# Performance work log

Measured on AMD Instinct MI355X. Metric: run time of the kernel, lower is better.

## Reference

```python
import jax, jax.numpy as jnp
import numpy as np

D_MODEL = 1024
NUM_HEADS = 16
HEAD_DIM = D_MODEL // NUM_HEADS  # 64
ROPE_BASE = 10000.0


def setup_inputs() -> dict:
    key = jax.random.key(0)
    ks = jax.random.split(key, 12)
    B, S, D = 4, 2048, D_MODEL
    scale = 1.0 / np.sqrt(D)
    inp = {
        'query': jax.random.normal(ks[0], (B, S, D), jnp.float32),
        'key': jax.random.normal(ks[1], (B, S, D), jnp.float32),
        'value': jax.random.normal(ks[2], (B, S, D), jnp.float32),
        'Wq': jax.random.normal(ks[3], (D, D), jnp.float32) * scale,
        'bq': jnp.zeros((D,), jnp.float32),
        'Wk': jax.random.normal(ks[4], (D, D), jnp.float32) * scale,
        'bk': jnp.zeros((D,), jnp.float32),
        'Wv': jax.random.normal(ks[5], (D, D), jnp.float32) * scale,
        'bv': jnp.zeros((D,), jnp.float32),
        'Wo': jax.random.normal(ks[6], (D, D), jnp.float32) * scale,
        'bo': jnp.zeros((D,), jnp.float32),
    }
    return inp


def _rope_cos_sin(seq_len, head_dim, dtype):
    inv_freq = 1.0 / (ROPE_BASE ** (jnp.arange(0, head_dim, 2, dtype=jnp.float32) / head_dim))
    t = jnp.arange(seq_len, dtype=jnp.float32)
    freqs = jnp.einsum('i,j->ij', t, inv_freq)          # [S, hd/2]
    emb = jnp.concatenate([freqs, freqs], axis=-1)      # [S, hd]
    return jnp.cos(emb).astype(dtype), jnp.sin(emb).astype(dtype)


def _rotate_half(x):
    x1, x2 = jnp.split(x, 2, axis=-1)
    return jnp.concatenate([-x2, x1], axis=-1)


def reference(query, key, value, Wq, bq, Wk, bk, Wv, bv, Wo, bo):
    B, T, D = query.shape
    H, hd = NUM_HEADS, HEAD_DIM
    # projections -> [B, H, S, hd]
    Q = (query @ Wq + bq).reshape(B, T, H, hd).transpose(0, 2, 1, 3)
    K = (key @ Wk + bk).reshape(B, -1, H, hd).transpose(0, 2, 1, 3)
    V = (value @ Wv + bv).reshape(B, -1, H, hd).transpose(0, 2, 1, 3)
    # RoPE
    cos, sin = _rope_cos_sin(T, hd, Q.dtype)            # [S, hd]
    Q = Q * cos + _rotate_half(Q) * sin
    K = K * cos + _rotate_half(K) * sin
    # attention
    scores = jnp.einsum('bhtd,bhsd->bhts', Q, K) / jnp.sqrt(jnp.asarray(hd, Q.dtype))
    attn = jax.nn.softmax(scores, axis=-1)
    context = jnp.einsum('bhts,bhsd->bhtd', attn, V)
    context = context.transpose(0, 2, 1, 3).reshape(B, T, D)
    return context @ Wo + bo
```

## Files before the change

### kernel.cpp

```cpp
#include <hip/hip_runtime.h>
#include <hip/hip_bf16.h>
#include <cstdint>
#include <cstddef>

typedef __bf16 bf16_t;
typedef __bf16 bf16x8 __attribute__((ext_vector_type(8)));
typedef __bf16 bf16x4v __attribute__((ext_vector_type(4)));
typedef __bf16 bf16x2v __attribute__((ext_vector_type(2)));
typedef float f32x4 __attribute__((ext_vector_type(4)));
typedef float f32x16 __attribute__((ext_vector_type(16)));
typedef uint32_t u32x4 __attribute__((ext_vector_type(4)));

#define DEVI static __device__ __forceinline__

DEVI void gl_lds16(const void* g, void* l) {
    __builtin_amdgcn_global_load_lds((const __attribute__((address_space(1))) void*)g,
                                     (__attribute__((address_space(3))) void*)l, 16, 0, 0);
}

DEVI float fexp2(float x) {
#if __has_builtin(__builtin_amdgcn_exp2f)
    return __builtin_amdgcn_exp2f(x);
#else
    return __expf(x * 0.6931471805599453f);
#endif
}

DEVI uint32_t pkbf16(float a, float b) {
    bf16x2v t;
    t[0] = (bf16_t)a;
    t[1] = (bf16_t)b;
    return __builtin_bit_cast(uint32_t, t);
}

__global__ __launch_bounds__(256) void castk(const float* __restrict__ i0, const float* __restrict__ i1,
                                             const float* __restrict__ i2, bf16_t* __restrict__ o0,
                                             bf16_t* __restrict__ o1, bf16_t* __restrict__ o2) {
    const float* in = blockIdx.y == 0 ? i0 : blockIdx.y == 1 ? i1 : i2;
    bf16_t* out = blockIdx.y == 0 ? o0 : blockIdx.y == 1 ? o1 : o2;
    size_t i = ((size_t)blockIdx.x * 256 + threadIdx.x) * 4;
    float4 v = *(const float4*)(in + i);
    bf16x4v o;
    o[0] = (bf16_t)v.x; o[1] = (bf16_t)v.y; o[2] = (bf16_t)v.z; o[3] = (bf16_t)v.w;
    *(bf16x4v*)(out + i) = o;
}

__global__ __launch_bounds__(256) void wtrans(const float* __restrict__ W0, const float* __restrict__ W1,
                                              const float* __restrict__ W2, const float* __restrict__ W3,
                                              bf16_t* __restrict__ O0, bf16_t* __restrict__ O1,
                                              bf16_t* __restrict__ O2, bf16_t* __restrict__ O3) {
    const float* W; bf16_t* O;
    switch (blockIdx.z) {
        case 0: W = W0; O = O0; break;
        case 1: W = W1; O = O1; break;
        case 2: W = W2; O = O2; break;
        default: W = W3; O = O3; break;
    }
    __shared__ float t[32][33];
    int tx = threadIdx.x & 31, ty = threadIdx.x >> 5;
    int bx = blockIdx.x * 32, by = blockIdx.y * 32;
#pragma unroll
    for (int yy = 0; yy < 4; ++yy)
        t[ty + yy * 8][tx] = W[(size_t)(by + ty + yy * 8) * 1024 + bx + tx];
    __syncthreads();
#pragma unroll
    for (int yy = 0; yy < 4; ++yy)
        O[(size_t)(bx + ty + yy * 8) * 1024 + by + tx] = (bf16_t)t[tx][ty + yy * 8];
}

__global__ __launch_bounds__(256) void rope_tab(float* __restrict__ ctab, float* __restrict__ stab) {
    int idx = blockIdx.x * 256 + threadIdx.x;
    int s = idx >> 5, i = idx & 31;
    float inv = 1.0f / powf(10000.0f, (float)i * (1.0f / 32.0f));
    float f = (float)s * inv;
    ctab[idx] = cosf(f);
    stab[idx] = sinf(f);
}

__global__ __launch_bounds__(256) void gemm_qkv(const bf16_t* __restrict__ Xq, const bf16_t* __restrict__ Xk,
                                                const bf16_t* __restrict__ Xv, const bf16_t* __restrict__ Wqt,
                                                const bf16_t* __restrict__ Wkt, const bf16_t* __restrict__ Wvt,
                                                const float* __restrict__ bqp, const float* __restrict__ bkp,
                                                const float* __restrict__ bvp, bf16_t* __restrict__ Qo,
                                                bf16_t* __restrict__ Ko, bf16_t* __restrict__ Vo,
                                                const float* __restrict__ ctab, const float* __restrict__ stab) {
    constexpr int K = 1024;
    const int z = blockIdx.z;
    const bf16_t* A  = z == 0 ? Xq : z == 1 ? Xk : Xv;
    const bf16_t* Bt = z == 0 ? Wqt : z == 1 ? Wkt : Wvt;
    const float* bias = z == 0 ? bqp : z == 1 ? bkp : bvp;
    bf16_t* O = z == 0 ? Qo : z == 1 ? Ko : Vo;
    const float scale = z == 0 ? 0.18033688011112042f : 1.0f;

    __shared__ alignas(16) bf16_t As[128 * 32];
    __shared__ alignas(16) bf16_t Bs[128 * 32];
    const int tid = threadIdx.x;
    const int w = tid >> 6, lane = tid & 63, c = lane & 15, qd = lane >> 4;
    const int wm = w >> 1, wn = w & 1;
    const int m0 = blockIdx.x * 128, n0 = blockIdx.y * 128;
    f32x4 acc[4][4] = {};
    for (int kt = 0; kt < K / 32; ++kt) {
#pragma unroll
        for (int l = 0; l < 2; ++l) {
            int e = (l * 256 + tid) * 8;
            int row = e >> 5, col = e & 31;
            gl_lds16(A + (size_t)(m0 + row) * K + kt * 32 + col, (char*)As + (size_t)e * 2);
            gl_lds16(Bt + (size_t)(n0 + row) * K + kt * 32 + col, (char*)Bs + (size_t)e * 2);
        }
        __syncthreads();
        bf16x8 af[4], bfr[4];
#pragma unroll
        for (int i = 0; i < 4; ++i) af[i] = *(const bf16x8*)&As[(wm * 64 + i * 16 + c) * 32 + qd * 8];
#pragma unroll
        for (int j = 0; j < 4; ++j) bfr[j] = *(const bf16x8*)&Bs[(wn * 64 + j * 16 + c) * 32 + qd * 8];
#pragma unroll
        for (int i = 0; i < 4; ++i)
#pragma unroll
            for (int j = 0; j < 4; ++j)
                acc[i][j] = __builtin_amdgcn_mfma_f32_16x16x32_bf16(af[i], bfr[j], acc[i][j], 0, 0, 0);
        __syncthreads();
    }
    const int mb = m0 + wm * 64;
    const int nb = n0 + wn * 64;
    const int h = nb >> 6;
    if (z == 2) {
#pragma unroll
        for (int i = 0; i < 4; ++i) {
            int m = mb + i * 16 + qd * 4;
            int b = m >> 11, s = m & 2047;
#pragma unroll
            for (int j = 0; j < 4; ++j) {
                int d = j * 16 + c;
                float bv = bias[nb + d];
                bf16x4v v4;
#pragma unroll
                for (int r = 0; r < 4; ++r) v4[r] = (bf16_t)(acc[i][j][r] + bv);
                *(bf16x4v*)(O + ((size_t)(b * 16 + h) * 64 + d) * 2048 + s) = v4;
            }
        }
    } else {
#pragma unroll
        for (int i = 0; i < 4; ++i)
#pragma unroll
            for (int jh = 0; jh < 2; ++jh) {
                int d1 = jh * 16 + c;
                float b1 = bias[nb + d1];
                float b2 = bias[nb + d1 + 32];
#pragma unroll
                for (int r = 0; r < 4; ++r) {
                    int m = mb + i * 16 + qd * 4 + r;
                    int b = m >> 11, s = m & 2047;
                    float v1 = acc[i][jh][r] + b1;
                    float v2 = acc[i][jh + 2][r] + b2;
                    float ct = ctab[s * 32 + d1];
                    float st = stab[s * 32 + d1];
                    size_t base = ((size_t)(b * 16 + h) * 2048 + s) * 64;
                    O[base + d1]      = (bf16_t)((v1 * ct - v2 * st) * scale);
                    O[base + d1 + 32] = (bf16_t)((v2 * ct + v1 * st) * scale);
                }
            }
    }
}

__global__ __launch_bounds__(256) void gemm_out(const bf16_t* __restrict__ A, const bf16_t* __restrict__ Bt,
                                                const float* __restrict__ bias, float* __restrict__ O) {
    constexpr int K = 1024, N = 1024;
    __shared__ alignas(16) bf16_t As[128 * 32];
    __shared__ alignas(16) bf16_t Bs[128 * 32];
    const int tid = threadIdx.x;
    const int w = tid >> 6, lane = tid & 63, c = lane & 15, qd = lane >> 4;
    const int wm = w >> 1, wn = w & 1;
    const int m0 = blockIdx.x * 128, n0 = blockIdx.y * 128;
    f32x4 acc[4][4] = {};
    for (int kt = 0; kt < K / 32; ++kt) {
#pragma unroll
        for (int l = 0; l < 2; ++l) {
            int e = (l * 256 + tid) * 8;
            int row = e >> 5, col = e & 31;
            gl_lds16(A + (size_t)(m0 + row) * K + kt * 32 + col, (char*)As + (size_t)e * 2);
            gl_lds16(Bt + (size_t)(n0 + row) * K + kt * 32 + col, (char*)Bs + (size_t)e * 2);
        }
        __syncthreads();
        bf16x8 af[4], bfr[4];
#pragma unroll
        for (int i = 0; i < 4; ++i) af[i] = *(const bf16x8*)&As[(wm * 64 + i * 16 + c) * 32 + qd * 8];
#pragma unroll
        for (int j = 0; j < 4; ++j) bfr[j] = *(const bf16x8*)&Bs[(wn * 64 + j * 16 + c) * 32 + qd * 8];
#pragma unroll
        for (int i = 0; i < 4; ++i)
#pragma unroll
            for (int j = 0; j < 4; ++j)
                acc[i][j] = __builtin_amdgcn_mfma_f32_16x16x32_bf16(af[i], bfr[j], acc[i][j], 0, 0, 0);
        __syncthreads();
    }
    const int mb = m0 + wm * 64, nb = n0 + wn * 64;
#pragma unroll
    for (int i = 0; i < 4; ++i)
#pragma unroll
        for (int j = 0; j < 4; ++j) {
            int n = nb + j * 16 + c;
            float bv = bias[n];
#pragma unroll
            for (int r = 0; r < 4; ++r) {
                int m = mb + i * 16 + qd * 4 + r;
                O[(size_t)m * N + n] = acc[i][j][r] + bv;
            }
        }
}

__global__ __launch_bounds__(256) void attn(const bf16_t* __restrict__ Q, const bf16_t* __restrict__ K,
                                            const bf16_t* __restrict__ Vt, bf16_t* __restrict__ ctx) {
    constexpr int S = 2048;
    __shared__ alignas(16) char smem[32768];
    const int tid = threadIdx.x, w = tid >> 6, lane = tid & 63;
    const int lo5 = lane & 31, hi = lane >> 5;
    const int rm = (lo5 >> 1) & 7;
    const int bh = blockIdx.x, q0 = blockIdx.y * 256;
    const bf16_t* Qb = Q + (size_t)bh * S * 64 + (size_t)q0 * 64;
    const bf16_t* Kb = K + (size_t)bh * S * 64;
    const bf16_t* Vb = Vt + (size_t)bh * 64 * S;
#pragma unroll
    for (int l = 0; l < 8; ++l) {
        int slot = l * 256 + tid;
        int row = slot >> 3, ch = slot & 7;
        int sch = ch ^ ((row >> 1) & 7);
        gl_lds16(Qb + (size_t)row * 64 + sch * 8, smem + (size_t)slot * 16);
    }
    __syncthreads();
    bf16x8 qf[4][2];
    {
        const bf16_t* Qs = (const bf16_t*)smem;
#pragma unroll
        for (int kc = 0; kc < 4; ++kc)
#pragma unroll
            for (int qb = 0; qb < 2; ++qb)
                qf[kc][qb] = *(const bf16x8*)&Qs[(size_t)(w * 64 + qb * 32 + lo5) * 64 + ((kc * 2 + hi) ^ rm) * 8];
    }
    __syncthreads();
    auto stageKV = [&](int kt, int buf) {
        const int s0 = kt * 64;
        char* kbase = smem + buf * 16384;
        char* vbase = kbase + 8192;
#pragma unroll
        for (int l = 0; l < 2; ++l) {
            int slot = l * 256 + tid;
            int row = slot >> 3, ch = slot & 7;
            int sch = ch ^ ((row >> 1) & 7);
            gl_lds16(Kb + (size_t)(s0 + row) * 64 + sch * 8, kbase + (size_t)slot * 16);
            gl_lds16(Vb + (size_t)row * S + s0 + sch * 8, vbase + (size_t)slot * 16);
        }
    };
    stageKV(0, 0);
    f32x16 acc_o[2][2] = {};
    f32x16 acc_l[2] = {};
    const f32x16 Z16 = {};
    bf16x8 ones;
    {
        u32x4 ov = {0x3F803F80u, 0x3F803F80u, 0x3F803F80u, 0x3F803F80u};
        ones = __builtin_bit_cast(bf16x8, ov);
    }
    __syncthreads();
    for (int kt = 0; kt < S / 64; ++kt) {
        const int cur = kt & 1;
        if (kt + 1 < S / 64) stageKV(kt + 1, cur ^ 1);
        const bf16_t* KsC = (const bf16_t*)(smem + cur * 16384);
        const bf16_t* VsC = (const bf16_t*)(smem + cur * 16384 + 8192);
        f32x16 st[2][2];
#pragma unroll
        for (int kc = 0; kc < 4; ++kc) {
            bf16x8 kf[2];
#pragma unroll
            for (int sb = 0; sb < 2; ++sb)
                kf[sb] = *(const bf16x8*)&KsC[(size_t)(sb * 32 + lo5) * 64 + ((kc * 2 + hi) ^ rm) * 8];
#pragma unroll
            for (int sb = 0; sb < 2; ++sb)
#pragma unroll
                for (int qb = 0; qb < 2; ++qb)
                    st[sb][qb] = __builtin_amdgcn_mfma_f32_32x32x16_bf16(kf[sb], qf[kc][qb],
                                                                         kc == 0 ? Z16 : st[sb][qb], 0, 0, 0);
        }
        uint32_t pku[2][2][8];
#pragma unroll
        for (int sb = 0; sb < 2; ++sb)
#pragma unroll
            for (int qb = 0; qb < 2; ++qb)
#pragma unroll
                for (int u = 0; u < 8; ++u)
                    pku[sb][qb][u] = pkbf16(fexp2(st[sb][qb][2 * u]), fexp2(st[sb][qb][2 * u + 1]));
#pragma unroll
        for (int skc = 0; skc < 4; ++skc) {
            bf16x8 vf[2];
#pragma unroll
            for (int db = 0; db < 2; ++db)
                vf[db] = *(const bf16x8*)&VsC[(size_t)(db * 32 + lo5) * 64 + ((skc * 2 + hi) ^ rm) * 8];
            const int sb = skc >> 1, b = (skc & 1) * 4;
#pragma unroll
            for (int qb = 0; qb < 2; ++qb) {
                uint32_t p0 = pku[sb][qb][b + 0], p1 = pku[sb][qb][b + 1];
                uint32_t p2 = pku[sb][qb][b + 2], p3 = pku[sb][qb][b + 3];
                uint32_t send0 = hi ? p0 : p2;
                uint32_t send1 = hi ? p1 : p3;
                uint32_t recv0 = __shfl_xor(send0, 32);
                uint32_t recv1 = __shfl_xor(send1, 32);
                u32x4 av = {hi ? recv0 : p0, hi ? recv1 : p1,
                            hi ? p2 : recv0, hi ? p3 : recv1};
                bf16x8 af = __builtin_bit_cast(bf16x8, av);
                acc_l[qb] = __builtin_amdgcn_mfma_f32_32x32x16_bf16(af, ones, acc_l[qb], 0, 0, 0);
#pragma unroll
                for (int db = 0; db < 2; ++db)
                    acc_o[qb][db] = __builtin_amdgcn_mfma_f32_32x32x16_bf16(af, vf[db], acc_o[qb][db], 0, 0, 0);
            }
        }
        __syncthreads();
    }
    const int b = bh >> 4, h = bh & 15;
#pragma unroll
    for (int qb = 0; qb < 2; ++qb) {
        float linv[16];
#pragma unroll
        for (int r = 0; r < 16; ++r) linv[r] = 1.0f / acc_l[qb][r];
#pragma unroll
        for (int db = 0; db < 2; ++db)
#pragma unroll
            for (int r = 0; r < 16; ++r) {
                int qrow = q0 + w * 64 + qb * 32 + (r & 3) + 8 * (r >> 2) + 4 * hi;
                int d = db * 32 + lo5;
                float o = acc_o[qb][db][r] * linv[r];
                ctx[((size_t)(b * 2048 + qrow)) * 1024 + (size_t)h * 64 + d] = (bf16_t)o;
            }
    }
}

extern "C" void kernel_launch(void* const* d_in, const int* in_sizes, int n_in,
                              void* d_out, int out_size, void* d_ws, size_t ws_size,
                              hipStream_t stream) {
    (void)in_sizes; (void)n_in; (void)out_size; (void)ws_size;
    const float* query = (const float*)d_in[0];
    const float* key   = (const float*)d_in[1];
    const float* value = (const float*)d_in[2];
    const float* Wq = (const float*)d_in[3];
    const float* bq = (const float*)d_in[4];
    const float* Wk = (const float*)d_in[5];
    const float* bk = (const float*)d_in[6];
    const float* Wv = (const float*)d_in[7];
    const float* bv = (const float*)d_in[8];
    const float* Wo = (const float*)d_in[9];
    const float* bo = (const float*)d_in[10];

    const size_t SZ = (size_t)8192 * 1024;
    bf16_t* Xq = (bf16_t*)d_ws;
    bf16_t* Xk = Xq + SZ;
    bf16_t* Xv = Xk + SZ;
    bf16_t* Qb = Xv + SZ;
    bf16_t* Kb = Qb + SZ;
    bf16_t* Vtb = Kb + SZ;
    bf16_t* Wqt = Vtb + SZ;
    bf16_t* Wkt = Wqt + 1024 * 1024;
    bf16_t* Wvt = Wkt + 1024 * 1024;
    bf16_t* Wot = Wvt + 1024 * 1024;
    float* ctab = (float*)(Wot + 1024 * 1024);
    float* stab = ctab + 2048 * 32;
    bf16_t* CT = Xq;

    castk<<<dim3(8192, 3), 256, 0, stream>>>(query, key, value, Xq, Xk, Xv);
    wtrans<<<dim3(32, 32, 4), 256, 0, stream>>>(Wq, Wk, Wv, Wo, Wqt, Wkt, Wvt, Wot);
    rope_tab<<<256, 256, 0, stream>>>(ctab, stab);
    gemm_qkv<<<dim3(64, 8, 3), 256, 0, stream>>>(Xq, Xk, Xv, Wqt, Wkt, Wvt, bq, bk, bv,
                                                 Qb, Kb, Vtb, ctab, stab);
    attn<<<dim3(64, 8), 256, 0, stream>>>(Qb, Kb, Vtb, CT);
    gemm_out<<<dim3(64, 8), 256, 0, stream>>>(CT, Wot, bo, (float*)d_out);
}
```

Before: 359.5 us.

## Halve attention query tile per block and use permlane32_swap for P exchange

The attention kernel now handles 128 query rows per block (32 per wave) instead of 256, which halves the per-wave accumulators and Q fragments and doubles the grid to 1024 blocks, with launch bounds requesting 4 blocks per CU. This is meant to raise occupancy and fill more CUs on the MI355X. In exchange, K/V tiles are streamed through LDS twice as often per query row, and each K/V fragment read feeds fewer MFMAs. The lane exchange of the P operand also uses the permlane32_swap builtin when available, replacing shuffles and selects.

```diff
diff --git a/kernel.cpp b/kernel.cpp
--- a/kernel.cpp
+++ b/kernel.cpp
@@ -10,6 +10,7 @@
 typedef float f32x4 __attribute__((ext_vector_type(4)));
 typedef float f32x16 __attribute__((ext_vector_type(16)));
 typedef uint32_t u32x4 __attribute__((ext_vector_type(4)));
+typedef uint32_t u32x2 __attribute__((ext_vector_type(2)));
 
 #define DEVI static __device__ __forceinline__
 
@@ -208,33 +209,31 @@
         }
 }
 
-__global__ __launch_bounds__(256) void attn(const bf16_t* __restrict__ Q, const bf16_t* __restrict__ K,
-                                            const bf16_t* __restrict__ Vt, bf16_t* __restrict__ ctx) {
+__global__ __launch_bounds__(256, 4) void attn(const bf16_t* __restrict__ Q, const bf16_t* __restrict__ K,
+                                               const bf16_t* __restrict__ Vt, bf16_t* __restrict__ ctx) {
     constexpr int S = 2048;
     __shared__ alignas(16) char smem[32768];
     const int tid = threadIdx.x, w = tid >> 6, lane = tid & 63;
     const int lo5 = lane & 31, hi = lane >> 5;
     const int rm = (lo5 >> 1) & 7;
-    const int bh = blockIdx.x, q0 = blockIdx.y * 256;
+    const int bh = blockIdx.x, q0 = blockIdx.y * 128;
     const bf16_t* Qb = Q + (size_t)bh * S * 64 + (size_t)q0 * 64;
     const bf16_t* Kb = K + (size_t)bh * S * 64;
     const bf16_t* Vb = Vt + (size_t)bh * 64 * S;
 #pragma unroll
-    for (int l = 0; l < 8; ++l) {
+    for (int l = 0; l < 4; ++l) {
         int slot = l * 256 + tid;
         int row = slot >> 3, ch = slot & 7;
         int sch = ch ^ ((row >> 1) & 7);
         gl_lds16(Qb + (size_t)row * 64 + sch * 8, smem + (size_t)slot * 16);
     }
     __syncthreads();
-    bf16x8 qf[4][2];
+    bf16x8 qf[4];
     {
         const bf16_t* Qs = (const bf16_t*)smem;
 #pragma unroll
         for (int kc = 0; kc < 4; ++kc)
-#pragma unroll
-            for (int qb = 0; qb < 2; ++qb)
-                qf[kc][qb] = *(const bf16x8*)&Qs[(size_t)(w * 64 + qb * 32 + lo5) * 64 + ((kc * 2 + hi) ^ rm) * 8];
+            qf[kc] = *(const bf16x8*)&Qs[(size_t)(w * 32 + lo5) * 64 + ((kc * 2 + hi) ^ rm) * 8];
     }
     __syncthreads();
     auto stageKV = [&](int kt, int buf) {
@@ -251,8 +250,8 @@
         }
     };
     stageKV(0, 0);
-    f32x16 acc_o[2][2] = {};
-    f32x16 acc_l[2] = {};
+    f32x16 acc_o[2] = {};
+    f32x16 acc_l = {};
     const f32x16 Z16 = {};
     bf16x8 ones;
     {
@@ -265,7 +264,7 @@
         if (kt + 1 < S / 64) stageKV(kt + 1, cur ^ 1);
         const bf16_t* KsC = (const bf16_t*)(smem + cur * 16384);
         const bf16_t* VsC = (const bf16_t*)(smem + cur * 16384 + 8192);
-        f32x16 st[2][2];
+        f32x16 st[2];
 #pragma unroll
         for (int kc = 0; kc < 4; ++kc) {
             bf16x8 kf[2];
@@ -274,19 +273,15 @@
                 kf[sb] = *(const bf16x8*)&KsC[(size_t)(sb * 32 + lo5) * 64 + ((kc * 2 + hi) ^ rm) * 8];
 #pragma unroll
             for (int sb = 0; sb < 2; ++sb)
-#pragma unroll
-                for (int qb = 0; qb < 2; ++qb)
-                    st[sb][qb] = __builtin_amdgcn_mfma_f32_32x32x16_bf16(kf[sb], qf[kc][qb],
-                                                                         kc == 0 ? Z16 : st[sb][qb], 0, 0, 0);
-        }
-        uint32_t pku[2][2][8];
+                st[sb] = __builtin_amdgcn_mfma_f32_32x32x16_bf16(kf[sb], qf[kc],
+                                                                 kc == 0 ? Z16 : st[sb], 0, 0, 0);
+        }
+        uint32_t pku[2][8];
 #pragma unroll
         for (int sb = 0; sb < 2; ++sb)
 #pragma unroll
-            for (int qb = 0; qb < 2; ++qb)
-#pragma unroll
-                for (int u = 0; u < 8; ++u)
-                    pku[sb][qb][u] = pkbf16(fexp2(st[sb][qb][2 * u]), fexp2(st[sb][qb][2 * u + 1]));
+            for (int u = 0; u < 8; ++u)
+                pku[sb][u] = pkbf16(fexp2(st[sb][2 * u]), fexp2(st[sb][2 * u + 1]));
 #pragma unroll
         for (int skc = 0; skc < 4; ++skc) {
             bf16x8 vf[2];
@@ -294,41 +289,41 @@
             for (int db = 0; db < 2; ++db)
                 vf[db] = *(const bf16x8*)&VsC[(size_t)(db * 32 + lo5) * 64 + ((skc * 2 + hi) ^ rm) * 8];
             const int sb = skc >> 1, b = (skc & 1) * 4;
-#pragma unroll
-            for (int qb = 0; qb < 2; ++qb) {
-                uint32_t p0 = pku[sb][qb][b + 0], p1 = pku[sb][qb][b + 1];
-                uint32_t p2 = pku[sb][qb][b + 2], p3 = pku[sb][qb][b + 3];
-                uint32_t send0 = hi ? p0 : p2;
-                uint32_t send1 = hi ? p1 : p3;
-                uint32_t recv0 = __shfl_xor(send0, 32);
-                uint32_t recv1 = __shfl_xor(send1, 32);
-                u32x4 av = {hi ? recv0 : p0, hi ? recv1 : p1,
-                            hi ? p2 : recv0, hi ? p3 : recv1};
-                bf16x8 af = __builtin_bit_cast(bf16x8, av);
-                acc_l[qb] = __builtin_amdgcn_mfma_f32_32x32x16_bf16(af, ones, acc_l[qb], 0, 0, 0);
-#pragma unroll
-                for (int db = 0; db < 2; ++db)
-                    acc_o[qb][db] = __builtin_amdgcn_mfma_f32_32x32x16_bf16(af, vf[db], acc_o[qb][db], 0, 0, 0);
-            }
+            uint32_t p0 = pku[sb][b + 0], p1 = pku[sb][b + 1];
+            uint32_t p2 = pku[sb][b + 2], p3 = pku[sb][b + 3];
+#if __has_builtin(__builtin_amdgcn_permlane32_swap)
+            u32x2 r02 = __builtin_amdgcn_permlane32_swap(p0, p2, false, false);
+            u32x2 r13 = __builtin_amdgcn_permlane32_swap(p1, p3, false, false);
+            u32x4 av = {r02[0], r13[0], r02[1], r13[1]};
+#else
+            uint32_t send0 = hi ? p0 : p2;
+            uint32_t send1 = hi ? p1 : p3;
+            uint32_t recv0 = __shfl_xor(send0, 32);
+            uint32_t recv1 = __shfl_xor(send1, 32);
+            u32x4 av = {hi ? recv0 : p0, hi ? recv1 : p1,
+                        hi ? p2 : recv0, hi ? p3 : recv1};
+#endif
+            bf16x8 af = __builtin_bit_cast(bf16x8, av);
+            acc_l = __builtin_amdgcn_mfma_f32_32x32x16_bf16(af, ones, acc_l, 0, 0, 0);
+#pragma unroll
+            for (int db = 0; db < 2; ++db)
+                acc_o[db] = __builtin_amdgcn_mfma_f32_32x32x16_bf16(af, vf[db], acc_o[db], 0, 0, 0);
         }
         __syncthreads();
     }
     const int b = bh >> 4, h = bh & 15;
-#pragma unroll
-    for (int qb = 0; qb < 2; ++qb) {
-        float linv[16];
-#pragma unroll
-        for (int r = 0; r < 16; ++r) linv[r] = 1.0f / acc_l[qb][r];
-#pragma unroll
-        for (int db = 0; db < 2; ++db)
-#pragma unroll
-            for (int r = 0; r < 16; ++r) {
-                int qrow = q0 + w * 64 + qb * 32 + (r & 3) + 8 * (r >> 2) + 4 * hi;
-                int d = db * 32 + lo5;
-                float o = acc_o[qb][db][r] * linv[r];
-                ctx[((size_t)(b * 2048 + qrow)) * 1024 + (size_t)h * 64 + d] = (bf16_t)o;
-            }
-    }
+    float linv[16];
+#pragma unroll
+    for (int r = 0; r < 16; ++r) linv[r] = 1.0f / acc_l[r];
+#pragma unroll
+    for (int db = 0; db < 2; ++db)
+#pragma unroll
+        for (int r = 0; r < 16; ++r) {
+            int qrow = q0 + w * 32 + (r & 3) + 8 * (r >> 2) + 4 * hi;
+            int d = db * 32 + lo5;
+            float o = acc_o[db][r] * linv[r];
+            ctx[((size_t)(b * 2048 + qrow)) * 1024 + (size_t)h * 64 + d] = (bf16_t)o;
+        }
 }
 
 extern "C" void kernel_launch(void* const* d_in, const int* in_sizes, int n_in,
@@ -367,6 +362,6 @@
     rope_tab<<<256, 256, 0, stream>>>(ctab, stab);
     gemm_qkv<<<dim3(64, 8, 3), 256, 0, stream>>>(Xq, Xk, Xv, Wqt, Wkt, Wvt, bq, bk, bv,
                                                  Qb, Kb, Vtb, ctab, stab);
-    attn<<<dim3(64, 8), 256, 0, stream>>>(Qb, Kb, Vtb, CT);
+    attn<<<dim3(64, 16), 256, 0, stream>>>(Qb, Kb, Vtb, CT);
     gemm_out<<<dim3(64, 8), 256, 0, stream>>>(CT, Wot, bo, (float*)d_out);
 }
```

New measurement: 341.6 us. -5.0%, faster.
